# Kernel optimization log

Hardware: AMD Instinct MI355X
Metric: run time of the kernel (lower is better)

## Reference

```python
import jax, jax.numpy as jnp
import numpy as np

B, T_Q, T_KV, D = 4, 2048, 4096, 1024
H = 16
HD = D // H  # head_dim = 64
EPS_LN = 1e-5
EPS_NORM = 1e-12


def setup_inputs() -> dict:
    key = jax.random.key(0)
    ks = jax.random.split(key, 12)
    inp = {
        'query': jax.random.normal(ks[0], (B, T_Q, D), jnp.float32),
        'key':   jax.random.normal(ks[1], (B, T_KV, D), jnp.float32),
        'value': jax.random.normal(ks[2], (B, T_KV, D), jnp.float32),
        # projections (nn.Linear stores weight as [out, in]; y = x @ W.T)
        'Wq': jax.random.normal(ks[3], (D, D), jnp.float32) * 0.02,
        'Wk': jax.random.normal(ks[4], (D, D), jnp.float32) * 0.02,
        'Wv': jax.random.normal(ks[5], (D, D), jnp.float32) * 0.02,
        'Wo': jax.random.normal(ks[6], (D, D), jnp.float32) * 0.01,
        'bo': jnp.zeros((D,), jnp.float32),
        'Wbeta':  jax.random.normal(ks[7], (H, D), jnp.float32) * 0.02,
        'bbeta':  jnp.zeros((H,), jnp.float32),
        'Walpha': jax.random.normal(ks[8], (H, D), jnp.float32) * 0.02,
        'balpha': jnp.full((H,), -1.0, jnp.float32),
        # per-head-dim LayerNorms
        'gq': jnp.ones((HD,), jnp.float32),
        'bq': jnp.zeros((HD,), jnp.float32),
        'gk': jnp.ones((HD,), jnp.float32),
        'bk': jnp.zeros((HD,), jnp.float32),
    }
    return inp


def _layernorm(x, g, b):
    mu = jnp.mean(x, axis=-1, keepdims=True)
    var = jnp.mean(jnp.square(x - mu), axis=-1, keepdims=True)
    return (x - mu) * jax.lax.rsqrt(var + EPS_LN) * g + b


def reference(query, key, value, Wq, Wk, Wv, Wo, bo,
              Wbeta, bbeta, Walpha, balpha, gq, bq, gk, bk):
    Bq, Tq, Dm = query.shape
    Tkv = key.shape[1]

    q = (query @ Wq.T).reshape(Bq, Tq, H, HD)
    k = (key   @ Wk.T).reshape(Bq, Tkv, H, HD)
    v = (value @ Wv.T).reshape(Bq, Tkv, H, HD)

    q = _layernorm(q, gq, bq)
    k = _layernorm(k, gk, bk)
    # F.normalize(k, dim=-1)
    k = k / jnp.maximum(jnp.linalg.norm(k, axis=-1, keepdims=True), EPS_NORM)

    beta  = jax.nn.sigmoid(key @ Wbeta.T  + bbeta)   # [B, Tkv, H]
    alpha = jax.nn.sigmoid(key @ Walpha.T + balpha)  # [B, Tkv, H]

    # time-major for scan: [Tkv, B, H, ...]
    k_t = jnp.moveaxis(k, 1, 0)
    v_t = jnp.moveaxis(v, 1, 0)
    b_t = jnp.moveaxis(beta, 1, 0)
    a_t = jnp.moveaxis(alpha, 1, 0)

    M0 = jnp.zeros((Bq, H, HD, HD), query.dtype)

    def step(M, inputs):
        kt, vt, bt, at = inputs  # [B,H,d],[B,H,d],[B,H],[B,H]
        Mk = jnp.einsum('bhij,bhj->bhi', M, kt)
        erase = at[..., None, None] * jnp.einsum('bhi,bhj->bhij', Mk, kt)
        write = bt[..., None, None] * jnp.einsum('bhi,bhj->bhij', vt, kt)
        return M - erase + write, None

    M, _ = jax.lax.scan(step, M0, (k_t, v_t, b_t, a_t))

    # out[b,t,h,i] = sum_j M[b,h,i,j] * q[b,t,h,j]
    out = jnp.einsum('bhij,bthj->bthi', M, q).reshape(Bq, Tq, Dm)
    out = out @ Wo.T + bo  # dropout is identity in eval mode
    return out
```

## Files before the change

kernel.cpp:

```cpp
#include <hip/hip_runtime.h>
#include <math.h>

#define TQ_LEN 2048
#define TKV_LEN 4096
#define BATCH 4
#define DMODEL 1024
#define NH 16
#define HD 64
#define NKBA 1280
#define CCH 128
#define NCHUNK (TKV_LEN / CCH)

typedef unsigned short u16;
typedef __attribute__((ext_vector_type(8))) short bf16x8;
typedef __attribute__((ext_vector_type(4))) float f32x4;

__device__ __forceinline__ u16 f2bf(float x) {
  union { float f; unsigned u; } c; c.f = x;
  unsigned r = c.u + 0x7fffu + ((c.u >> 16) & 1u);
  return (u16)(r >> 16);
}
__device__ __forceinline__ float bf2f(u16 x) {
  union { unsigned u; float f; } c; c.u = ((unsigned)x) << 16;
  return c.f;
}

__device__ __forceinline__ float wave_sum64(float x) {
#pragma unroll
  for (int off = 32; off; off >>= 1) x += __shfl_xor(x, off, 64);
  return x;
}

__global__ __launch_bounds__(256) void cvt_bf16_kernel(
    const float* __restrict__ s, u16* __restrict__ d) {
  size_t i = ((size_t)blockIdx.x * 256 + threadIdx.x) * 8;
  float4 a = *(const float4*)&s[i];
  float4 b = *(const float4*)&s[i + 4];
  union { u16 h[8]; uint4 v; } o;
  o.h[0] = f2bf(a.x); o.h[1] = f2bf(a.y); o.h[2] = f2bf(a.z); o.h[3] = f2bf(a.w);
  o.h[4] = f2bf(b.x); o.h[5] = f2bf(b.y); o.h[6] = f2bf(b.z); o.h[7] = f2bf(b.w);
  *(uint4*)&d[i] = o.v;
}

__global__ __launch_bounds__(256) void wcat_bf_kernel(
    const float* __restrict__ Wk, const float* __restrict__ Wb,
    const float* __restrict__ Wa, u16* __restrict__ Wcat) {
  int i = blockIdx.x * 256 + threadIdx.x;
  int row = i / DMODEL, col = i % DMODEL;
  float v;
  if (row < 1024)      v = Wk[i];
  else if (row < 1040) v = Wb[(row - 1024) * DMODEL + col];
  else if (row < 1056) v = Wa[(row - 1040) * DMODEL + col];
  else                 v = 0.f;
  Wcat[i] = f2bf(v);
}

#define BAR() __builtin_amdgcn_s_barrier()
#define PRIO(x) __builtin_amdgcn_s_setprio(x)
#define VMCNT(n)                                              \
  do {                                                        \
    __builtin_amdgcn_sched_barrier(0);                        \
    asm volatile("s_waitcnt vmcnt(" #n ")" ::: "memory");     \
  } while (0)
#define LGKM0()                                               \
  do {                                                        \
    asm volatile("s_waitcnt lgkmcnt(0)" ::: "memory");        \
    __builtin_amdgcn_sched_barrier(0);                        \
  } while (0)

__device__ __forceinline__ void stage128(
    const u16* __restrict__ G, int ldg, int row0, int kc,
    u16* ldsbase, int wid, int lane) {
#pragma unroll
  for (int e = 0; e < 2; ++e) {
    int j0 = wid * 64 + e * 512;
    int j = j0 + lane;
    int r = j >> 3;
    int cg = ((j & 7) ^ (r & 7)) * 8;
    const u16* g = G + (size_t)(row0 + r) * ldg + kc + cg;
    __builtin_amdgcn_global_load_lds(
        (const __attribute__((address_space(1))) void*)g,
        (__attribute__((address_space(3))) void*)(ldsbase + (size_t)j0 * 8),
        16, 0, 0);
  }
}

#define READ_A(L)                                                             \
  do {                                                                        \
    _Pragma("unroll") for (int mf = 0; mf < 4; ++mf)                          \
    _Pragma("unroll") for (int kk = 0; kk < 2; ++kk)                          \
      af[mf][kk] = *(const bf16x8*)&(L)[(wm * 64 + mf * 16 + lrow) * 64 +     \
                                        (((kk * 4 + (lane >> 4)) ^ xorg) * 8)];\
  } while (0)

#define READ_B(L, n_, dst)                                                    \
  do {                                                                        \
    _Pragma("unroll") for (int nf = 0; nf < 2; ++nf)                          \
    _Pragma("unroll") for (int kk = 0; kk < 2; ++kk)                          \
      dst[nf][kk] = *(const bf16x8*)&(L)[(wn * 64 + (n_) * 32 + nf * 16 +     \
                                          lrow) * 64 +                        \
                                         (((kk * 4 + (lane >> 4)) ^ xorg) * 8)];\
  } while (0)

#define MFMA_Q(n_, bfx)                                                       \
  do {                                                                        \
    _Pragma("unroll") for (int mf = 0; mf < 4; ++mf)                          \
    _Pragma("unroll") for (int nf = 0; nf < 2; ++nf)                          \
    _Pragma("unroll") for (int kk = 0; kk < 2; ++kk)                          \
      acc[mf][n_][nf] = __builtin_amdgcn_mfma_f32_16x16x32_bf16(              \
          af[mf][kk], bfx[nf][kk], acc[mf][n_][nf], 0, 0, 0);                 \
  } while (0)

template <bool HAS_BIAS, bool OUT_BF16>
__global__ __launch_bounds__(512, 2) void gemm_bt_128x256(
    const u16* __restrict__ A, const u16* __restrict__ B,
    const float* __restrict__ bias, void* __restrict__ Cv,
    int K, int ldc, int nbx) {
  __shared__ u16 lA[2][8192];
  __shared__ u16 lB[2][16384];
  const int tid = threadIdx.x;
  const int lane = tid & 63, wid = tid >> 6;
  const int wm = wid >> 2, wn = wid & 3;
  const int nwg = gridDim.x, cpx = nwg >> 3, orig = blockIdx.x;
  const int swz = (orig & 7) * cpx + (orig >> 3);
  const int bm = (swz / nbx) * 128, bn = (swz % nbx) * 256;
  const int lrow = lane & 15;
  const int xorg = lrow & 7;
  const int NT = K >> 6;

  f32x4 acc[4][2][2] = {};
  bf16x8 af[4][2], bf0[2][2], bf1[2][2];

  u16* lA0 = &lA[0][0]; u16* lA1 = &lA[1][0];
  u16* lB0 = &lB[0][0]; u16* lB1 = &lB[1][0];

  stage128(A, K, bm, 0, lA0, wid, lane);
  stage128(B, K, bn, 0, lB0, wid, lane);
  stage128(B, K, bn + 128, 0, lB0 + 8192, wid, lane);
  stage128(A, K, bm, 64, lA1, wid, lane);
  stage128(B, K, bn, 64, lB1, wid, lane);
  stage128(B, K, bn + 128, 64, lB1 + 8192, wid, lane);
  VMCNT(0);
  BAR();

  for (int i = 0; i < NT / 2; ++i) {
    const int t0 = 2 * i;
    const bool more = (t0 + 2) < NT;
    READ_A(lA0);
    READ_B(lB0, 0, bf0);
    READ_B(lB0, 1, bf1);
    BAR(); PRIO(1); MFMA_Q(0, bf0); PRIO(0); BAR();
    if (more) stage128(A, K, bm, (t0 + 2) * 64, lA0, wid, lane);
    BAR(); PRIO(1); MFMA_Q(1, bf1); PRIO(0);
    if (more) { VMCNT(2); } else { VMCNT(0); }
    BAR();
    READ_A(lA1);
    READ_B(lB1, 0, bf0);
    READ_B(lB1, 1, bf1);
    if (more) stage128(B, K, bn, (t0 + 2) * 64, lB0, wid, lane);
    BAR(); PRIO(1); MFMA_Q(0, bf0); PRIO(0);
    LGKM0();
    BAR();
    if (more) {
      stage128(B, K, bn + 128, (t0 + 2) * 64, lB0 + 8192, wid, lane);
      stage128(A, K, bm, (t0 + 3) * 64, lA1, wid, lane);
      stage128(B, K, bn, (t0 + 3) * 64, lB1, wid, lane);
      stage128(B, K, bn + 128, (t0 + 3) * 64, lB1 + 8192, wid, lane);
    }
    BAR(); PRIO(1); MFMA_Q(1, bf1); PRIO(0);
    VMCNT(6);
    BAR();
  }

#pragma unroll
  for (int n = 0; n < 2; ++n)
#pragma unroll
    for (int mf = 0; mf < 4; ++mf)
#pragma unroll
      for (int nf = 0; nf < 2; ++nf) {
        int col = bn + wn * 64 + n * 32 + nf * 16 + (lane & 15);
        float bv = HAS_BIAS ? bias[col] : 0.f;
        int row0 = bm + wm * 64 + mf * 16 + (lane >> 4) * 4;
#pragma unroll
        for (int ii = 0; ii < 4; ++ii) {
          float vout = acc[mf][n][nf][ii] + bv;
          if (OUT_BF16)
            ((u16*)Cv)[(size_t)(row0 + ii) * ldc + col] = f2bf(vout);
          else
            ((float*)Cv)[(size_t)(row0 + ii) * ldc + col] = vout;
        }
      }
}

__global__ __launch_bounds__(256) void ln_q_kernel(float* __restrict__ q,
                                                   const float* __restrict__ g,
                                                   const float* __restrict__ b) {
  int gidx = blockIdx.x * 4 + (threadIdx.x >> 6);
  int lane = threadIdx.x & 63;
  int row = gidx >> 4, h = gidx & 15;
  float* p = q + (size_t)row * DMODEL + h * HD + lane;
  float x = *p;
  float mu = wave_sum64(x) * (1.f / 64.f);
  float d = x - mu;
  float var = wave_sum64(d * d) * (1.f / 64.f);
  float y = d * rsqrtf(var + 1e-5f) * g[lane] + b[lane];
  *p = y;
}

__global__ __launch_bounds__(256) void ln_k_kernel(float* __restrict__ kb,
                                                   const float* __restrict__ g,
                                                   const float* __restrict__ b) {
  int gidx = blockIdx.x * 4 + (threadIdx.x >> 6);
  int lane = threadIdx.x & 63;
  int row = gidx >> 4, h = gidx & 15;
  float* p = kb + (size_t)row * NKBA + h * HD + lane;
  float x = *p;
  float mu = wave_sum64(x) * (1.f / 64.f);
  float d = x - mu;
  float var = wave_sum64(d * d) * (1.f / 64.f);
  float y = d * rsqrtf(var + 1e-5f) * g[lane] + b[lane];
  float s2 = wave_sum64(y * y);
  y = y / fmaxf(sqrtf(s2), 1e-12f);
  *p = y;
}

__global__ __launch_bounds__(256) void sig_kernel(
    const float* __restrict__ kb, const float* __restrict__ bb,
    const float* __restrict__ ba, float* __restrict__ beta,
    float* __restrict__ alpha) {
  int i = blockIdx.x * 256 + threadIdx.x;
  int row = i >> 4, h = i & 15;
  float lb = kb[(size_t)row * NKBA + 1024 + h] + bb[h];
  float la = kb[(size_t)row * NKBA + 1040 + h] + ba[h];
  beta[i]  = 1.f / (1.f + expf(-lb));
  alpha[i] = 1.f / (1.f + expf(-la));
}

__global__ __launch_bounds__(64, 2) void chunk_scan_kernel(
    const float* __restrict__ kb, const u16* __restrict__ v,
    const float* __restrict__ beta, const float* __restrict__ alpha,
    float* __restrict__ Pbuf, float* __restrict__ Sbuf) {
  __shared__ float klds[2][64];
  int slot = blockIdx.x;
  int bh = slot / NCHUNK, ck = slot % NCHUNK;
  int b = bh >> 4, h = bh & 15;
  int lane = threadIdx.x;
  int t0 = ck * CCH;
  const float* kbase = kb + ((size_t)b * TKV_LEN + t0) * NKBA + h * HD;
  const u16* vbase = v + ((size_t)b * TKV_LEN + t0) * DMODEL + h * HD;
  const float* bbase = beta + ((size_t)b * TKV_LEN + t0) * NH + h;
  const float* abase = alpha + ((size_t)b * TKV_LEN + t0) * NH + h;

  float P[64], S[64];
#pragma unroll
  for (int j = 0; j < 64; ++j) { P[j] = (j == lane) ? 1.f : 0.f; S[j] = 0.f; }

  klds[0][lane] = kbase[lane];
  float kn = kbase[(size_t)NKBA + lane];
  float vn = bf2f(vbase[lane]);
  float btn = bbase[0];
  float atn = abase[0];

  for (int t = 0; t < CCH; ++t) {
    float vc = vn, bt = btn, at = atn;
    if (t + 1 < CCH) {
      vn = bf2f(vbase[(size_t)(t + 1) * DMODEL + lane]);
      btn = bbase[(size_t)(t + 1) * NH];
      atn = abase[(size_t)(t + 1) * NH];
    }
    klds[(t + 1) & 1][lane] = kn;
    kn = (t + 2 < CCH) ? kbase[(size_t)(t + 2) * NKBA + lane] : 0.f;
    const float* kcur = klds[t & 1];
    float pk0 = 0.f, pk1 = 0.f, sk0 = 0.f, sk1 = 0.f;
#pragma unroll
    for (int g = 0; g < 4; ++g) {
      float4 ka = *(const float4*)&kcur[g * 16 + 0];
      float4 kc = *(const float4*)&kcur[g * 16 + 4];
      float4 ke = *(const float4*)&kcur[g * 16 + 8];
      float4 kg = *(const float4*)&kcur[g * 16 + 12];
      pk0 = fmaf(P[g*16+ 0], ka.x, pk0); pk1 = fmaf(P[g*16+ 1], ka.y, pk1);
      pk0 = fmaf(P[g*16+ 2], ka.z, pk0); pk1 = fmaf(P[g*16+ 3], ka.w, pk1);
      pk0 = fmaf(P[g*16+ 4], kc.x, pk0); pk1 = fmaf(P[g*16+ 5], kc.y, pk1);
      pk0 = fmaf(P[g*16+ 6], kc.z, pk0); pk1 = fmaf(P[g*16+ 7], kc.w, pk1);
      pk0 = fmaf(P[g*16+ 8], ke.x, pk0); pk1 = fmaf(P[g*16+ 9], ke.y, pk1);
      pk0 = fmaf(P[g*16+10], ke.z, pk0); pk1 = fmaf(P[g*16+11], ke.w, pk1);
      pk0 = fmaf(P[g*16+12], kg.x, pk0); pk1 = fmaf(P[g*16+13], kg.y, pk1);
      pk0 = fmaf(P[g*16+14], kg.z, pk0); pk1 = fmaf(P[g*16+15], kg.w, pk1);
      sk0 = fmaf(S[g*16+ 0], ka.x, sk0); sk1 = fmaf(S[g*16+ 1], ka.y, sk1);
      sk0 = fmaf(S[g*16+ 2], ka.z, sk0); sk1 = fmaf(S[g*16+ 3], ka.w, sk1);
      sk0 = fmaf(S[g*16+ 4], kc.x, sk0); sk1 = fmaf(S[g*16+ 5], kc.y, sk1);
      sk0 = fmaf(S[g*16+ 6], kc.z, sk0); sk1 = fmaf(S[g*16+ 7], kc.w, sk1);
      sk0 = fmaf(S[g*16+ 8], ke.x, sk0); sk1 = fmaf(S[g*16+ 9], ke.y, sk1);
      sk0 = fmaf(S[g*16+10], ke.z, sk0); sk1 = fmaf(S[g*16+11], ke.w, sk1);
      sk0 = fmaf(S[g*16+12], kg.x, sk0); sk1 = fmaf(S[g*16+13], kg.y, sk1);
      sk0 = fmaf(S[g*16+14], kg.z, sk0); sk1 = fmaf(S[g*16+15], kg.w, sk1);
    }
    float cp = -at * (pk0 + pk1);
    float cs = fmaf(bt, vc, -at * (sk0 + sk1));
#pragma unroll
    for (int g = 0; g < 4; ++g) {
      float4 ka = *(const float4*)&kcur[g * 16 + 0];
      float4 kc = *(const float4*)&kcur[g * 16 + 4];
      float4 ke = *(const float4*)&kcur[g * 16 + 8];
      float4 kg = *(const float4*)&kcur[g * 16 + 12];
      P[g*16+ 0] = fmaf(cp, ka.x, P[g*16+ 0]); P[g*16+ 1] = fmaf(cp, ka.y, P[g*16+ 1]);
      P[g*16+ 2] = fmaf(cp, ka.z, P[g*16+ 2]); P[g*16+ 3] = fmaf(cp, ka.w, P[g*16+ 3]);
      P[g*16+ 4] = fmaf(cp, kc.x, P[g*16+ 4]); P[g*16+ 5] = fmaf(cp, kc.y, P[g*16+ 5]);
      P[g*16+ 6] = fmaf(cp, kc.z, P[g*16+ 6]); P[g*16+ 7] = fmaf(cp, kc.w, P[g*16+ 7]);
      P[g*16+ 8] = fmaf(cp, ke.x, P[g*16+ 8]); P[g*16+ 9] = fmaf(cp, ke.y, P[g*16+ 9]);
      P[g*16+10] = fmaf(cp, ke.z, P[g*16+10]); P[g*16+11] = fmaf(cp, ke.w, P[g*16+11]);
      P[g*16+12] = fmaf(cp, kg.x, P[g*16+12]); P[g*16+13] = fmaf(cp, kg.y, P[g*16+13]);
      P[g*16+14] = fmaf(cp, kg.z, P[g*16+14]); P[g*16+15] = fmaf(cp, kg.w, P[g*16+15]);
      S[g*16+ 0] = fmaf(cs, ka.x, S[g*16+ 0]); S[g*16+ 1] = fmaf(cs, ka.y, S[g*16+ 1]);
      S[g*16+ 2] = fmaf(cs, ka.z, S[g*16+ 2]); S[g*16+ 3] = fmaf(cs, ka.w, S[g*16+ 3]);
      S[g*16+ 4] = fmaf(cs, kc.x, S[g*16+ 4]); S[g*16+ 5] = fmaf(cs, kc.y, S[g*16+ 5]);
      S[g*16+ 6] = fmaf(cs, kc.z, S[g*16+ 6]); S[g*16+ 7] = fmaf(cs, kc.w, S[g*16+ 7]);
      S[g*16+ 8] = fmaf(cs, ke.x, S[g*16+ 8]); S[g*16+ 9] = fmaf(cs, ke.y, S[g*16+ 9]);
      S[g*16+10] = fmaf(cs, ke.z, S[g*16+10]); S[g*16+11] = fmaf(cs, ke.w, S[g*16+11]);
      S[g*16+12] = fmaf(cs, kg.x, S[g*16+12]); S[g*16+13] = fmaf(cs, kg.y, S[g*16+13]);
      S[g*16+14] = fmaf(cs, kg.z, S[g*16+14]); S[g*16+15] = fmaf(cs, kg.w, S[g*16+15]);
    }
  }
  float* po = Pbuf + (size_t)slot * 4096 + (size_t)lane * 64;
  float* so = Sbuf + (size_t)slot * 4096 + (size_t)lane * 64;
#pragma unroll
  for (int j4 = 0; j4 < 16; ++j4) {
    *(float4*)&po[j4 * 4] = make_float4(P[4 * j4], P[4 * j4 + 1], P[4 * j4 + 2], P[4 * j4 + 3]);
    *(float4*)&so[j4 * 4] = make_float4(S[4 * j4], S[4 * j4 + 1], S[4 * j4 + 2], S[4 * j4 + 3]);
  }
}

__global__ __launch_bounds__(256) void fold_kernel(
    const float* __restrict__ Pin, const float* __restrict__ Sin,
    float* __restrict__ Pout, float* __restrict__ Sout, int nitems) {
  __shared__ float Pa[64][68], Sa[64][68], Pc[64][68], Sc[64][68];
  const int tid = threadIdx.x;
  const int r0 = (tid >> 4) * 4, c0 = (tid & 15) * 4;
  for (int l = tid; l < 4096; l += 256) {
    int r = l >> 6, c = l & 63;
    Pa[r][c] = (r == c) ? 1.f : 0.f;
    Sa[r][c] = 0.f;
  }
  for (int item = 0; item < nitems; ++item) {
    const float* pg = Pin + ((size_t)blockIdx.x * nitems + item) * 4096;
    const float* sg = Sin + ((size_t)blockIdx.x * nitems + item) * 4096;
#pragma unroll
    for (int e = 0; e < 4; ++e) {
      int l = tid * 16 + e * 4;
      int r = l >> 6, c = l & 63;
      *(float4*)&Pc[r][c] = *(const float4*)&pg[l];
      *(float4*)&Sc[r][c] = *(const float4*)&sg[l];
    }
    __syncthreads();
    float accP[4][4] = {}, accS[4][4] = {};
#pragma unroll 4
    for (int j4 = 0; j4 < 16; ++j4) {
      float bmat[4][4];
#pragma unroll
      for (int jj = 0; jj < 4; ++jj) {
        float4 t = *(const float4*)&Pc[j4 * 4 + jj][c0];
        bmat[jj][0] = t.x; bmat[jj][1] = t.y; bmat[jj][2] = t.z; bmat[jj][3] = t.w;
      }
#pragma unroll
      for (int rr = 0; rr < 4; ++rr) {
        float4 tp = *(const float4*)&Pa[r0 + rr][j4 * 4];
        float4 ts = *(const float4*)&Sa[r0 + rr][j4 * 4];
        float ap[4] = {tp.x, tp.y, tp.z, tp.w};
        float as[4] = {ts.x, ts.y, ts.z, ts.w};
#pragma unroll
        for (int jj = 0; jj < 4; ++jj)
#pragma unroll
          for (int cc = 0; cc < 4; ++cc) {
            accP[rr][cc] = fmaf(ap[jj], bmat[jj][cc], accP[rr][cc]);
            accS[rr][cc] = fmaf(as[jj], bmat[jj][cc], accS[rr][cc]);
          }
      }
    }
#pragma unroll
    for (int rr = 0; rr < 4; ++rr)
#pragma unroll
      for (int cc = 0; cc < 4; ++cc) accS[rr][cc] += Sc[r0 + rr][c0 + cc];
    __syncthreads();
#pragma unroll
    for (int rr = 0; rr < 4; ++rr)
#pragma unroll
      for (int cc = 0; cc < 4; ++cc) {
        Pa[r0 + rr][c0 + cc] = accP[rr][cc];
        Sa[r0 + rr][c0 + cc] = accS[rr][cc];
      }
  }
  __syncthreads();
  float* po = Pout + (size_t)blockIdx.x * 4096;
  float* so = Sout + (size_t)blockIdx.x * 4096;
#pragma unroll
  for (int e = 0; e < 4; ++e) {
    int l = tid * 16 + e * 4;
    int r = l >> 6, c = l & 63;
    *(float4*)&po[l] = *(const float4*)&Pa[r][c];
    *(float4*)&so[l] = *(const float4*)&Sa[r][c];
  }
}

__global__ __launch_bounds__(256) void outm_kernel(
    const float* __restrict__ Mg, const float* __restrict__ q,
    u16* __restrict__ attn) {
  __shared__ float Ml[64][65];
  int bh = blockIdx.x;
  int tchunk = blockIdx.y;
  int b = bh >> 4, h = bh & 15;
  int tid = threadIdx.x;
  const float* mg = Mg + (size_t)bh * 4096;
#pragma unroll
  for (int e = 0; e < 16; ++e) {
    int l = tid + e * 256;
    Ml[l >> 6][l & 63] = mg[l];
  }
  __syncthreads();
  int lane = tid & 63, tt = tid >> 6;
  const float* qb = q + ((size_t)b * TQ_LEN + tchunk * 256) * DMODEL + h * HD;
  u16* ob = attn + ((size_t)b * TQ_LEN + tchunk * 256) * DMODEL + h * HD;
  for (int it = 0; it < 64; ++it) {
    int t = it * 4 + tt;
    const float* qr = qb + (size_t)t * DMODEL;
    float acc = 0.f;
#pragma unroll
    for (int j4 = 0; j4 < 16; ++j4) {
      float4 qv = *(const float4*)&qr[j4 * 4];
      acc += Ml[lane][j4 * 4 + 0] * qv.x + Ml[lane][j4 * 4 + 1] * qv.y +
             Ml[lane][j4 * 4 + 2] * qv.z + Ml[lane][j4 * 4 + 3] * qv.w;
    }
    ob[(size_t)t * DMODEL + lane] = f2bf(acc);
  }
}

extern "C" void kernel_launch(void* const* d_in, const int* in_sizes, int n_in,
                              void* d_out, int out_size, void* d_ws,
                              size_t ws_size, hipStream_t stream) {
  const float* query = (const float*)d_in[0];
  const float* key   = (const float*)d_in[1];
  const float* value = (const float*)d_in[2];
  const float* Wq    = (const float*)d_in[3];
  const float* Wk    = (const float*)d_in[4];
  const float* Wv    = (const float*)d_in[5];
  const float* Wo    = (const float*)d_in[6];
  const float* bo    = (const float*)d_in[7];
  const float* Wbeta = (const float*)d_in[8];
  const float* bbeta = (const float*)d_in[9];
  const float* Walpha= (const float*)d_in[10];
  const float* balpha= (const float*)d_in[11];
  const float* gq    = (const float*)d_in[12];
  const float* bq    = (const float*)d_in[13];
  const float* gk    = (const float*)d_in[14];
  const float* bk    = (const float*)d_in[15];
  float* out = (float*)d_out;

  const int MQ = BATCH * TQ_LEN;
  const int MKV = BATCH * TKV_LEN;
  const int NSLOT = 64 * NCHUNK;

  float* ws = (float*)d_ws;
  size_t off = 0;
  u16* Wcat_bf = (u16*)(ws + off); off += (size_t)NKBA * DMODEL / 2;
  u16* Wq_bf   = (u16*)(ws + off); off += (size_t)DMODEL * DMODEL / 2;
  u16* Wv_bf   = (u16*)(ws + off); off += (size_t)DMODEL * DMODEL / 2;
  u16* Wo_bf   = (u16*)(ws + off); off += (size_t)DMODEL * DMODEL / 2;
  u16* qbf = (u16*)(ws + off); size_t qbf_f = off; off += (size_t)MQ * DMODEL / 2;
  u16* kbf = (u16*)(ws + off); size_t kbf_f = off; off += (size_t)MKV * DMODEL / 2;
  u16* vbf = (u16*)(ws + off); size_t vbf_f = off; off += (size_t)MKV * DMODEL / 2;
  float* qp   = ws + off; off += (size_t)MQ * DMODEL;
  float* kba  = ws + off; size_t kba_f = off; off += (size_t)MKV * NKBA;
  u16* vpb = (u16*)(ws + off); off += (size_t)MKV * DMODEL / 2;
  float* Pbuf = ws + kbf_f;
  float* Sbuf = ws + vbf_f;
  float* Gp   = ws + qbf_f;
  float* Gs   = ws + qbf_f + 1048576;
  float* Fp   = ws + qbf_f + 2097152;
  float* beta = ws + qbf_f + 2359296;
  float* alpha= ws + qbf_f + 2621440;
  float* Mg   = ws + qbf_f + 2883584;
  u16* attn_bf = (u16*)(ws + kba_f);

  wcat_bf_kernel<<<NKBA * DMODEL / 256, 256, 0, stream>>>(Wk, Wbeta, Walpha, Wcat_bf);
  cvt_bf16_kernel<<<DMODEL * DMODEL / 2048, 256, 0, stream>>>(Wq, Wq_bf);
  cvt_bf16_kernel<<<DMODEL * DMODEL / 2048, 256, 0, stream>>>(Wv, Wv_bf);
  cvt_bf16_kernel<<<DMODEL * DMODEL / 2048, 256, 0, stream>>>(Wo, Wo_bf);
  cvt_bf16_kernel<<<MQ * DMODEL / 2048, 256, 0, stream>>>(query, qbf);
  cvt_bf16_kernel<<<MKV * DMODEL / 2048, 256, 0, stream>>>(key, kbf);
  cvt_bf16_kernel<<<MKV * DMODEL / 2048, 256, 0, stream>>>(value, vbf);
  gemm_bt_128x256<false, false><<<(DMODEL / 256) * (MQ / 128), 512, 0, stream>>>(
      qbf, Wq_bf, nullptr, qp, DMODEL, DMODEL, DMODEL / 256);
  gemm_bt_128x256<false, false><<<(NKBA / 256) * (MKV / 128), 512, 0, stream>>>(
      kbf, Wcat_bf, nullptr, kba, DMODEL, NKBA, NKBA / 256);
  gemm_bt_128x256<false, true><<<(DMODEL / 256) * (MKV / 128), 512, 0, stream>>>(
      vbf, Wv_bf, nullptr, vpb, DMODEL, DMODEL, DMODEL / 256);
  ln_q_kernel<<<MQ * NH / 4, 256, 0, stream>>>(qp, gq, bq);
  ln_k_kernel<<<MKV * NH / 4, 256, 0, stream>>>(kba, gk, bk);
  sig_kernel<<<MKV * NH / 256, 256, 0, stream>>>(kba, bbeta, balpha, beta, alpha);
  chunk_scan_kernel<<<NSLOT, 64, 0, stream>>>(kba, vpb, beta, alpha, Pbuf, Sbuf);
  fold_kernel<<<NSLOT / 8, 256, 0, stream>>>(Pbuf, Sbuf, Gp, Gs, 8);
  fold_kernel<<<64, 256, 0, stream>>>(Gp, Gs, Fp, Mg, 4);
  outm_kernel<<<dim3(64, TQ_LEN / 256), 256, 0, stream>>>(Mg, qp, attn_bf);
  gemm_bt_128x256<true, false><<<(DMODEL / 256) * (MQ / 128), 512, 0, stream>>>(
      attn_bf, Wo_bf, bo, out, DMODEL, DMODEL, DMODEL / 256);
  (void)in_sizes; (void)n_in; (void)out_size; (void)ws_size;
}
```

Baseline: 588.3 us.

## Halve scan chunk length and store per-chunk transition matrices in bf16

Shrinks the chunk length of the chunked delta-rule scan from 128 to 64, doubling the number of parallel chunk blocks and halving the sequential steps each block runs. The per-chunk P/S matrices are now written as bf16, and a new fold kernel reads and widens them, which limits the growth in intermediate memory traffic. Two fold levels (8 then 8) reduce the larger chunk count. Risks are extra fold work and precision loss from storing the chunk transition matrices in bf16. The Gs buffer is moved to the end of the workspace to fit the larger intermediates.

```diff
diff --git a/kernel.cpp b/kernel.cpp
--- a/kernel.cpp
+++ b/kernel.cpp
@@ -8,7 +8,7 @@
 #define NH 16
 #define HD 64
 #define NKBA 1280
-#define CCH 128
+#define CCH 64
 #define NCHUNK (TKV_LEN / CCH)
 
 typedef unsigned short u16;
@@ -239,7 +239,7 @@
 __global__ __launch_bounds__(64, 2) void chunk_scan_kernel(
     const float* __restrict__ kb, const u16* __restrict__ v,
     const float* __restrict__ beta, const float* __restrict__ alpha,
-    float* __restrict__ Pbuf, float* __restrict__ Sbuf) {
+    u16* __restrict__ Pbuf, u16* __restrict__ Sbuf) {
   __shared__ float klds[2][64];
   int slot = blockIdx.x;
   int bh = slot / NCHUNK, ck = slot % NCHUNK;
@@ -321,12 +321,97 @@
       S[g*16+14] = fmaf(cs, kg.z, S[g*16+14]); S[g*16+15] = fmaf(cs, kg.w, S[g*16+15]);
     }
   }
-  float* po = Pbuf + (size_t)slot * 4096 + (size_t)lane * 64;
-  float* so = Sbuf + (size_t)slot * 4096 + (size_t)lane * 64;
-#pragma unroll
-  for (int j4 = 0; j4 < 16; ++j4) {
-    *(float4*)&po[j4 * 4] = make_float4(P[4 * j4], P[4 * j4 + 1], P[4 * j4 + 2], P[4 * j4 + 3]);
-    *(float4*)&so[j4 * 4] = make_float4(S[4 * j4], S[4 * j4 + 1], S[4 * j4 + 2], S[4 * j4 + 3]);
+  u16* po = Pbuf + (size_t)slot * 4096 + (size_t)lane * 64;
+  u16* so = Sbuf + (size_t)slot * 4096 + (size_t)lane * 64;
+#pragma unroll
+  for (int j8 = 0; j8 < 8; ++j8) {
+    union { u16 h[8]; uint4 v4; } op, os;
+#pragma unroll
+    for (int e = 0; e < 8; ++e) {
+      op.h[e] = f2bf(P[j8 * 8 + e]);
+      os.h[e] = f2bf(S[j8 * 8 + e]);
+    }
+    *(uint4*)&po[j8 * 8] = op.v4;
+    *(uint4*)&so[j8 * 8] = os.v4;
+  }
+}
+
+__global__ __launch_bounds__(256) void fold_bf_kernel(
+    const u16* __restrict__ Pin, const u16* __restrict__ Sin,
+    float* __restrict__ Pout, float* __restrict__ Sout, int nitems) {
+  __shared__ float Pa[64][68], Sa[64][68], Pc[64][68], Sc[64][68];
+  const int tid = threadIdx.x;
+  const int r0 = (tid >> 4) * 4, c0 = (tid & 15) * 4;
+  for (int l = tid; l < 4096; l += 256) {
+    int r = l >> 6, c = l & 63;
+    Pa[r][c] = (r == c) ? 1.f : 0.f;
+    Sa[r][c] = 0.f;
+  }
+  for (int item = 0; item < nitems; ++item) {
+    const u16* pg = Pin + ((size_t)blockIdx.x * nitems + item) * 4096;
+    const u16* sg = Sin + ((size_t)blockIdx.x * nitems + item) * 4096;
+#pragma unroll
+    for (int e = 0; e < 4; ++e) {
+      int l = tid * 16 + e * 4;
+      int r = l >> 6, c = l & 63;
+      uint2 rp = *(const uint2*)&pg[l];
+      uint2 rs = *(const uint2*)&sg[l];
+      Pc[r][c + 0] = bf2f((u16)(rp.x & 0xffffu));
+      Pc[r][c + 1] = bf2f((u16)(rp.x >> 16));
+      Pc[r][c + 2] = bf2f((u16)(rp.y & 0xffffu));
+      Pc[r][c + 3] = bf2f((u16)(rp.y >> 16));
+      Sc[r][c + 0] = bf2f((u16)(rs.x & 0xffffu));
+      Sc[r][c + 1] = bf2f((u16)(rs.x >> 16));
+      Sc[r][c + 2] = bf2f((u16)(rs.y & 0xffffu));
+      Sc[r][c + 3] = bf2f((u16)(rs.y >> 16));
+    }
+    __syncthreads();
+    float accP[4][4] = {}, accS[4][4] = {};
+#pragma unroll 4
+    for (int j4 = 0; j4 < 16; ++j4) {
+      float bmat[4][4];
+#pragma unroll
+      for (int jj = 0; jj < 4; ++jj) {
+        float4 t = *(const float4*)&Pc[j4 * 4 + jj][c0];
+        bmat[jj][0] = t.x; bmat[jj][1] = t.y; bmat[jj][2] = t.z; bmat[jj][3] = t.w;
+      }
+#pragma unroll
+      for (int rr = 0; rr < 4; ++rr) {
+        float4 tp = *(const float4*)&Pa[r0 + rr][j4 * 4];
+        float4 ts = *(const float4*)&Sa[r0 + rr][j4 * 4];
+        float ap[4] = {tp.x, tp.y, tp.z, tp.w};
+        float as[4] = {ts.x, ts.y, ts.z, ts.w};
+#pragma unroll
+        for (int jj = 0; jj < 4; ++jj)
+#pragma unroll
+          for (int cc = 0; cc < 4; ++cc) {
+            accP[rr][cc] = fmaf(ap[jj], bmat[jj][cc], accP[rr][cc]);
+            accS[rr][cc] = fmaf(as[jj], bmat[jj][cc], accS[rr][cc]);
+          }
+      }
+    }
+#pragma unroll
+    for (int rr = 0; rr < 4; ++rr)
+#pragma unroll
+      for (int cc = 0; cc < 4; ++cc) accS[rr][cc] += Sc[r0 + rr][c0 + cc];
+    __syncthreads();
+#pragma unroll
+    for (int rr = 0; rr < 4; ++rr)
+#pragma unroll
+      for (int cc = 0; cc < 4; ++cc) {
+        Pa[r0 + rr][c0 + cc] = accP[rr][cc];
+        Sa[r0 + rr][c0 + cc] = accS[rr][cc];
+      }
+  }
+  __syncthreads();
+  float* po = Pout + (size_t)blockIdx.x * 4096;
+  float* so = Sout + (size_t)blockIdx.x * 4096;
+#pragma unroll
+  for (int e = 0; e < 4; ++e) {
+    int l = tid * 16 + e * 4;
+    int r = l >> 6, c = l & 63;
+    *(float4*)&po[l] = *(const float4*)&Pa[r][c];
+    *(float4*)&so[l] = *(const float4*)&Sa[r][c];
   }
 }
 
@@ -470,14 +555,14 @@
   float* qp   = ws + off; off += (size_t)MQ * DMODEL;
   float* kba  = ws + off; size_t kba_f = off; off += (size_t)MKV * NKBA;
   u16* vpb = (u16*)(ws + off); off += (size_t)MKV * DMODEL / 2;
-  float* Pbuf = ws + kbf_f;
-  float* Sbuf = ws + vbf_f;
+  u16* Pbuf_bf = (u16*)(ws + kbf_f);
+  u16* Sbuf_bf = (u16*)(ws + vbf_f);
   float* Gp   = ws + qbf_f;
-  float* Gs   = ws + qbf_f + 1048576;
   float* Fp   = ws + qbf_f + 2097152;
   float* beta = ws + qbf_f + 2359296;
   float* alpha= ws + qbf_f + 2621440;
   float* Mg   = ws + qbf_f + 2883584;
+  float* Gs   = ws + off;
   u16* attn_bf = (u16*)(ws + kba_f);
 
   wcat_bf_kernel<<<NKBA * DMODEL / 256, 256, 0, stream>>>(Wk, Wbeta, Walpha, Wcat_bf);
@@ -496,9 +581,9 @@
   ln_q_kernel<<<MQ * NH / 4, 256, 0, stream>>>(qp, gq, bq);
   ln_k_kernel<<<MKV * NH / 4, 256, 0, stream>>>(kba, gk, bk);
   sig_kernel<<<MKV * NH / 256, 256, 0, stream>>>(kba, bbeta, balpha, beta, alpha);
-  chunk_scan_kernel<<<NSLOT, 64, 0, stream>>>(kba, vpb, beta, alpha, Pbuf, Sbuf);
-  fold_kernel<<<NSLOT / 8, 256, 0, stream>>>(Pbuf, Sbuf, Gp, Gs, 8);
-  fold_kernel<<<64, 256, 0, stream>>>(Gp, Gs, Fp, Mg, 4);
+  chunk_scan_kernel<<<NSLOT, 64, 0, stream>>>(kba, vpb, beta, alpha, Pbuf_bf, Sbuf_bf);
+  fold_bf_kernel<<<NSLOT / 8, 256, 0, stream>>>(Pbuf_bf, Sbuf_bf, Gp, Gs, 8);
+  fold_kernel<<<64, 256, 0, stream>>>(Gp, Gs, Fp, Mg, 8);
   outm_kernel<<<dim3(64, TQ_LEN / 256), 256, 0, stream>>>(Mg, qp, attn_bf);
   gemm_bt_128x256<true, false><<<(DMODEL / 256) * (MQ / 128), 512, 0, stream>>>(
       attn_bf, Wo_bf, bo, out, DMODEL, DMODEL, DMODEL / 256);
```

Result: slower. 621.8 us (+5.7%).
